# Performance work log

Measured on AMD Instinct MI355X. Metric: run time of the kernel, lower is better.

## Reference

```python
import jax, jax.numpy as jnp
import numpy as np

B, S, D, H = 2, 2048, 1024, 16  # batch, seq_len, model dim, heads


def setup_inputs() -> dict:
    key = jax.random.key(0)
    ks = jax.random.split(key, 5)
    return {
        "x": jax.random.normal(ks[0], (B, S, D), jnp.float32),
        "idx": jax.random.randint(ks[1], (B,), 0, S),
        "weight": jnp.float32(0.5),
        "attn_forcing": 1,  # static python flag
        "w_qkv": jax.random.normal(ks[2], (D, 3 * D), jnp.float32) * 0.02,
        "b_qkv": jnp.zeros((3 * D,), jnp.float32),
        "w_proj": jax.random.normal(ks[3], (D, D), jnp.float32) * 0.02,
        "b_proj": jnp.zeros((D,), jnp.float32),
    }


def reference(x, idx, weight, attn_forcing, w_qkv, b_qkv, w_proj, b_proj):
    Bx, Sx, Dm = x.shape
    dh = Dm // H
    # qkv projection (Conv1D: x @ w + b)
    qkv = x @ w_qkv + b_qkv  # [B,S,3D]
    q, k, v = jnp.split(qkv, 3, axis=-1)
    q = q.reshape(Bx, Sx, H, dh).transpose(0, 2, 1, 3)  # [B,H,S,dh]
    k = k.reshape(Bx, Sx, H, dh).transpose(0, 2, 1, 3)
    v = v.reshape(Bx, Sx, H, dh).transpose(0, 2, 1, 3)
    alen = jnp.arange(Sx)
    mask = (alen[None, :] <= alen[:, None]).astype(x.dtype)  # [S,S] causal
    w = jnp.einsum('bhqd,bhkd->bhqk', q, k) / jnp.asarray(np.sqrt(dh), x.dtype)
    w = w * mask + jnp.asarray(-1e9, x.dtype) * (1 - mask)
    w = jax.nn.softmax(w, axis=-1)
    if attn_forcing:
        # post-softmax forcing reweight: positions >= idx scaled by weight, then renorm
        a = jnp.where(alen[None, :] >= idx[:, None], weight, jnp.asarray(1.0, x.dtype))  # [B,S]
        w = w * a[:, None, None, :]
        w = w / jnp.sum(w, axis=-1, keepdims=True)
    out = jnp.einsum('bhqk,bhkd->bhqd', w, v)  # [B,H,S,dh]
    out = out.transpose(0, 2, 1, 3).reshape(Bx, Sx, Dm)  # merge heads
    return out @ w_proj + b_proj
```

## Files before the change

kernel.cpp:

```cpp
#include <hip/hip_runtime.h>


typedef __attribute__((ext_vector_type(8))) short short8;
typedef __attribute__((ext_vector_type(4))) float f32x4;

#define MFMA_B16(a, b, c) __builtin_amdgcn_mfma_f32_16x16x32_bf16(a, b, c, 0, 0, 0)

static __device__ __forceinline__ unsigned short f2bf(float f) {
    union { float f; unsigned int u; } v;
    v.f = f;
    unsigned int r = (v.u + 0x7fffu + ((v.u >> 16) & 1u)) >> 16;
    return (unsigned short)r;
}

static __device__ __forceinline__ unsigned int pk_bf16(float a, float b) {
#if __has_builtin(__builtin_amdgcn_cvt_pk_bf16_f32)
    typedef __bf16 bf2 __attribute__((ext_vector_type(2)));
    union { bf2 v; unsigned int u; } c;
    c.v = __builtin_amdgcn_cvt_pk_bf16_f32(a, b);
    return c.u;
#else
    return (unsigned int)f2bf(a) | ((unsigned int)f2bf(b) << 16);
#endif
}

static __device__ __forceinline__ void gl_lds16(const void* g, void* l) {
    __builtin_amdgcn_global_load_lds(
        (const __attribute__((address_space(1))) unsigned int*)g,
        (__attribute__((address_space(3))) unsigned int*)l, 16, 0, 0);
}

__global__ __launch_bounds__(256) void convert_x_kernel(const float4* __restrict__ x,
                                                        ushort4* __restrict__ xb) {
    int i = blockIdx.x * 256 + threadIdx.x;
    float4 v = x[i];
    ushort4 o;
    o.x = f2bf(v.x); o.y = f2bf(v.y); o.z = f2bf(v.z); o.w = f2bf(v.w);
    xb[i] = o;
}

__global__ __launch_bounds__(256) void transpose_cvt_kernel(const float* __restrict__ in,
                                                            unsigned short* __restrict__ out,
                                                            int R, int C) {
    __shared__ float t[32][33];
    int c0 = blockIdx.x * 32, r0 = blockIdx.y * 32;
    int x = threadIdx.x, y = threadIdx.y;
    #pragma unroll
    for (int yy = y; yy < 32; yy += 8)
        t[yy][x] = in[(size_t)(r0 + yy) * C + (c0 + x)];
    __syncthreads();
    #pragma unroll
    for (int yy = y; yy < 32; yy += 8)
        out[(size_t)(c0 + yy) * R + (r0 + x)] = f2bf(t[x][yy]);
}

__global__ __launch_bounds__(256) void transpose_v_kernel(const unsigned short* __restrict__ v,
                                                          unsigned short* __restrict__ vT) {
    __shared__ unsigned short t[32][33];
    int d0 = blockIdx.x * 32, s0 = blockIdx.y * 32, bh = blockIdx.z;
    const unsigned short* vb = v + (size_t)bh * 2048 * 64;
    unsigned short* vTb = vT + (size_t)bh * 2048 * 64;
    int x = threadIdx.x, y = threadIdx.y;
    #pragma unroll
    for (int yy = y; yy < 32; yy += 8)
        t[yy][x] = vb[(s0 + yy) * 64 + d0 + x];
    __syncthreads();
    #pragma unroll
    for (int yy = y; yy < 32; yy += 8)
        vTb[(d0 + yy) * 2048 + s0 + x] = t[x][yy];
}

__global__ __launch_bounds__(256) void gemm_qkv_kernel(const unsigned short* __restrict__ A,
                                                       const unsigned short* __restrict__ Bt,
                                                       const float* __restrict__ bias,
                                                       unsigned short* __restrict__ q,
                                                       unsigned short* __restrict__ k,
                                                       unsigned short* __restrict__ v) {
    __shared__ unsigned short As[128 * 64];
    __shared__ unsigned short Bs[128 * 64];
    const int tid = threadIdx.x;
    const int lane = tid & 63, wave = tid >> 6;
    const int l15 = lane & 15, quad = lane >> 4;
    const int wm = wave >> 1, wn = wave & 1;
    const int row0 = blockIdx.y * 128, col0 = blockIdx.x * 128;
    const int K = 1024;

    int srow[4], scol[4], sdst[4];
    #pragma unroll
    for (int h = 0; h < 4; ++h) {
        int D = h * 256 + wave * 64 + lane;
        srow[h] = D >> 3;
        scol[h] = ((D & 7) ^ (srow[h] & 7)) * 8;
        sdst[h] = (h * 256 + wave * 64) * 8;
    }

    f32x4 acc[4][4] = {};

    for (int kt = 0; kt < K; kt += 64) {
        #pragma unroll
        for (int h = 0; h < 4; ++h) {
            gl_lds16(&A[(size_t)(row0 + srow[h]) * K + kt + scol[h]], &As[sdst[h]]);
            gl_lds16(&Bt[(size_t)(col0 + srow[h]) * K + kt + scol[h]], &Bs[sdst[h]]);
        }
        __syncthreads();
        #pragma unroll
        for (int kk = 0; kk < 2; ++kk) {
            short8 af[4], bf[4];
            #pragma unroll
            for (int i = 0; i < 4; ++i) {
                int r = wm * 64 + i * 16 + l15;
                af[i] = *(const short8*)&As[r * 64 + (((kk * 4 + quad) ^ (r & 7)) * 8)];
            }
            #pragma unroll
            for (int j = 0; j < 4; ++j) {
                int r = wn * 64 + j * 16 + l15;
                bf[j] = *(const short8*)&Bs[r * 64 + (((kk * 4 + quad) ^ (r & 7)) * 8)];
            }
            #pragma unroll
            for (int i = 0; i < 4; ++i)
                #pragma unroll
                for (int j = 0; j < 4; ++j)
                    acc[i][j] = MFMA_B16(af[i], bf[j], acc[i][j]);
        }
        __syncthreads();
    }

    #pragma unroll
    for (int i = 0; i < 4; ++i)
        #pragma unroll
        for (int j = 0; j < 4; ++j)
            #pragma unroll
            for (int r = 0; r < 4; ++r) {
                int row = row0 + wm * 64 + i * 16 + quad * 4 + r;
                int col = col0 + wn * 64 + j * 16 + l15;
                float val = acc[i][j][r] + bias[col];
                int which = col >> 10, rem = col & 1023;
                int hh = rem >> 6, d = rem & 63;
                int b = row >> 11, s = row & 2047;
                size_t o = ((size_t)((b * 16 + hh) * 2048 + s)) * 64 + d;
                if (which == 0) q[o] = f2bf(val * 0.125f);
                else if (which == 1) k[o] = f2bf(val);
                else v[o] = f2bf(val);
            }
}

__global__ __launch_bounds__(256) void gemm_proj_kernel(const unsigned short* __restrict__ A,
                                                        const unsigned short* __restrict__ Bt,
                                                        const float* __restrict__ bias,
                                                        float* __restrict__ out) {
    __shared__ unsigned short As[128 * 64];
    __shared__ unsigned short Bs[64 * 64];
    const int tid = threadIdx.x;
    const int lane = tid & 63, wave = tid >> 6;
    const int l15 = lane & 15, quad = lane >> 4;
    const int wm = wave >> 1, wn = wave & 1;
    const int row0 = blockIdx.y * 128, col0 = blockIdx.x * 64;
    const int K = 1024;

    int srow[4], scol[4], sdst[4];
    #pragma unroll
    for (int h = 0; h < 4; ++h) {
        int D = h * 256 + wave * 64 + lane;
        srow[h] = D >> 3;
        scol[h] = ((D & 7) ^ (srow[h] & 7)) * 8;
        sdst[h] = (h * 256 + wave * 64) * 8;
    }

    f32x4 acc[4][2] = {};

    for (int kt = 0; kt < K; kt += 64) {
        #pragma unroll
        for (int h = 0; h < 4; ++h)
            gl_lds16(&A[(size_t)(row0 + srow[h]) * K + kt + scol[h]], &As[sdst[h]]);
        #pragma unroll
        for (int h = 0; h < 2; ++h)
            gl_lds16(&Bt[(size_t)(col0 + srow[h]) * K + kt + scol[h]], &Bs[sdst[h]]);
        __syncthreads();
        #pragma unroll
        for (int kk = 0; kk < 2; ++kk) {
            short8 af[4], bf[2];
            #pragma unroll
            for (int i = 0; i < 4; ++i) {
                int r = wm * 64 + i * 16 + l15;
                af[i] = *(const short8*)&As[r * 64 + (((kk * 4 + quad) ^ (r & 7)) * 8)];
            }
            #pragma unroll
            for (int j = 0; j < 2; ++j) {
                int r = wn * 32 + j * 16 + l15;
                bf[j] = *(const short8*)&Bs[r * 64 + (((kk * 4 + quad) ^ (r & 7)) * 8)];
            }
            #pragma unroll
            for (int i = 0; i < 4; ++i)
                #pragma unroll
                for (int j = 0; j < 2; ++j)
                    acc[i][j] = MFMA_B16(af[i], bf[j], acc[i][j]);
        }
        __syncthreads();
    }

    #pragma unroll
    for (int i = 0; i < 4; ++i)
        #pragma unroll
        for (int j = 0; j < 2; ++j)
            #pragma unroll
            for (int r = 0; r < 4; ++r) {
                int row = row0 + wm * 64 + i * 16 + quad * 4 + r;
                int col = col0 + wn * 32 + j * 16 + l15;
                out[(size_t)row * 1024 + col] = acc[i][j][r] + bias[col];
            }
}

__global__ __launch_bounds__(256) void attn_kernel(const unsigned short* __restrict__ Q,
                                                   const unsigned short* __restrict__ Kg,
                                                   const unsigned short* __restrict__ Vt,
                                                   const int* __restrict__ idx,
                                                   const float* __restrict__ weight,
                                                   const int* __restrict__ forcing,
                                                   unsigned short* __restrict__ O) {
    __shared__ unsigned short Ks[2][4096];
    __shared__ unsigned short Vs[2][4096];

    const int tid = threadIdx.x;
    const int lane = tid & 63, wave = tid >> 6;
    const int l15 = lane & 15, quad = lane >> 4;
    const int bid = blockIdx.x;
    const int u = bid >> 5, a = u & 7, qg = u >> 3;
    const int t = (qg == 0) ? (31 - a) : (qg == 1) ? (16 + a) : (qg == 2) ? (15 - a) : a;
    const int bh = bid & 31;
    const int b = bh >> 4, hh = bh & 15;
    const unsigned short* Qb = Q + (size_t)bh * 2048 * 64;
    const unsigned short* Kh = Kg + (size_t)bh * 2048 * 64;
    const unsigned short* Vh = Vt + (size_t)bh * 2048 * 64;

    const int idxb = idx[b];
    const float wgt = (forcing[0] != 0) ? weight[0] : 1.0f;

    const int L0 = wave * 128 + lane;
    const int rS = L0 >> 3;
    const int cS = (L0 & 7) ^ (rS & 7);
    const int ldsOffJ0 = (wave * 128) * 8;
    const int ldsOffJ1 = (wave * 128 + 64) * 8;

    const int q0 = t * 64 + wave * 16;
    const int qrow = q0 + l15;

    short8 aq0 = *(const short8*)&Qb[(q0 + l15) * 64 + quad * 8];
    short8 aq1 = *(const short8*)&Qb[(q0 + l15) * 64 + 32 + quad * 8];

    float m = -3.0e38f, l = 0.0f;
    f32x4 o[4] = {};

    const int nkb = t + 1;

    {
        const unsigned short* kg = Kh + (size_t)rS * 64 + cS * 8;
        const unsigned short* vg = Vh + (size_t)rS * 2048 + cS * 8;
        gl_lds16(kg,            &Ks[0][ldsOffJ0]);
        gl_lds16(kg + 8 * 64,   &Ks[0][ldsOffJ1]);
        gl_lds16(vg,            &Vs[0][ldsOffJ0]);
        gl_lds16(vg + 8 * 2048, &Vs[0][ldsOffJ1]);
    }
    __syncthreads();

    for (int kb = 0; kb < nkb; ++kb) {
        const int cur = kb & 1;
        const int kbase = kb * 64;
        if (kb + 1 < nkb) {
            const int nb = kbase + 64;
            const unsigned short* kg = Kh + (size_t)(nb + rS) * 64 + cS * 8;
            const unsigned short* vg = Vh + (size_t)rS * 2048 + nb + cS * 8;
            gl_lds16(kg,            &Ks[cur ^ 1][ldsOffJ0]);
            gl_lds16(kg + 8 * 64,   &Ks[cur ^ 1][ldsOffJ1]);
            gl_lds16(vg,            &Vs[cur ^ 1][ldsOffJ0]);
            gl_lds16(vg + 8 * 2048, &Vs[cur ^ 1][ldsOffJ1]);
        }

        f32x4 sT[4];
        #pragma unroll
        for (int kt = 0; kt < 4; ++kt) {
            const int row = kt * 16 + l15;
            short8 k0 = *(const short8*)&Ks[cur][row * 64 + ((quad ^ (row & 7)) * 8)];
            short8 k1 = *(const short8*)&Ks[cur][row * 64 + (((4 + quad) ^ (row & 7)) * 8)];
            f32x4 z = {};
            z = MFMA_B16(k0, aq0, z);
            z = MFMA_B16(k1, aq1, z);
            sT[kt] = z;
        }

        if (kb == t) {
            #pragma unroll
            for (int kt = 0; kt < 4; ++kt)
                #pragma unroll
                for (int r = 0; r < 4; ++r)
                    if (kbase + kt * 16 + quad * 4 + r > qrow) sT[kt][r] = -3.0e38f;
        }

        float mloc = fmaxf(fmaxf(fmaxf(sT[0][0], sT[0][1]), fmaxf(sT[0][2], sT[0][3])),
                           fmaxf(fmaxf(sT[1][0], sT[1][1]), fmaxf(sT[1][2], sT[1][3])));
        mloc = fmaxf(mloc, fmaxf(fmaxf(fmaxf(sT[2][0], sT[2][1]), fmaxf(sT[2][2], sT[2][3])),
                                 fmaxf(fmaxf(sT[3][0], sT[3][1]), fmaxf(sT[3][2], sT[3][3]))));
        mloc = fmaxf(mloc, __shfl_xor(mloc, 16));
        mloc = fmaxf(mloc, __shfl_xor(mloc, 32));
        const float mnew = fmaxf(m, mloc);
        const float alpha = __expf(m - mnew);
        m = mnew;

        #pragma unroll
        for (int kt = 0; kt < 4; ++kt)
            #pragma unroll
            for (int r = 0; r < 4; ++r)
                sT[kt][r] = __expf(sT[kt][r] - mnew);
        if (kbase >= idxb) {
            #pragma unroll
            for (int kt = 0; kt < 4; ++kt)
                #pragma unroll
                for (int r = 0; r < 4; ++r) sT[kt][r] *= wgt;
        } else if (kbase + 63 >= idxb) {
            #pragma unroll
            for (int kt = 0; kt < 4; ++kt)
                #pragma unroll
                for (int r = 0; r < 4; ++r)
                    if (kbase + kt * 16 + quad * 4 + r >= idxb) sT[kt][r] *= wgt;
        }

        float rs = ((sT[0][0] + sT[0][1]) + (sT[0][2] + sT[0][3])) +
                   ((sT[1][0] + sT[1][1]) + (sT[1][2] + sT[1][3])) +
                   ((sT[2][0] + sT[2][1]) + (sT[2][2] + sT[2][3])) +
                   ((sT[3][0] + sT[3][1]) + (sT[3][2] + sT[3][3]));
        rs += __shfl_xor(rs, 16);
        rs += __shfl_xor(rs, 32);
        l = l * alpha + rs;

        #pragma unroll
        for (int dt = 0; dt < 4; ++dt) {
            f32x4 tt = o[dt];
            #pragma unroll
            for (int r = 0; r < 4; ++r) tt[r] *= alpha;
            o[dt] = tt;
        }

        unsigned int plo[4], phi[4];
        #pragma unroll
        for (int kt = 0; kt < 4; ++kt) {
            plo[kt] = pk_bf16(sT[kt][0], sT[kt][1]);
            phi[kt] = pk_bf16(sT[kt][2], sT[kt][3]);
        }

        #pragma unroll
        for (int ka = 0; ka < 2; ++ka) {
            const int srcA = ((quad & 1) * 32) + l15;
            const int srcB = srcA + 16;
            unsigned int tA0 = __shfl(plo[ka * 2], srcA), tA1 = __shfl(plo[ka * 2 + 1], srcA);
            unsigned int hA0 = __shfl(phi[ka * 2], srcA), hA1 = __shfl(phi[ka * 2 + 1], srcA);
            unsigned int tB0 = __shfl(plo[ka * 2], srcB), tB1 = __shfl(plo[ka * 2 + 1], srcB);
            unsigned int hB0 = __shfl(phi[ka * 2], srcB), hB1 = __shfl(phi[ka * 2 + 1], srcB);
            const bool hi = quad >= 2;
            union { short8 v; unsigned int u[4]; } pf;
            pf.u[0] = hi ? tA1 : tA0;
            pf.u[1] = hi ? hA1 : hA0;
            pf.u[2] = hi ? tB1 : tB0;
            pf.u[3] = hi ? hB1 : hB0;
            #pragma unroll
            for (int dt = 0; dt < 4; ++dt) {
                const int row = dt * 16 + l15;
                short8 vf = *(const short8*)&Vs[cur][row * 64 + (((ka * 4 + quad) ^ (row & 7)) * 8)];
                o[dt] = MFMA_B16(vf, pf.v, o[dt]);
            }
        }

        __syncthreads();
    }

    const float inv = 1.0f / l;
    unsigned short* sc = &Ks[0][0] + wave * 1152;
    #pragma unroll
    for (int dt = 0; dt < 4; ++dt)
        #pragma unroll
        for (int r = 0; r < 4; ++r)
            sc[l15 * 72 + dt * 16 + quad * 4 + r] = f2bf(o[dt][r] * inv);
    const size_t rowoff = ((size_t)(b * 2048 + q0 + l15)) * 1024 + hh * 64;
    #pragma unroll
    for (int h = 0; h < 2; ++h) {
        short8 v8 = *(const short8*)&sc[l15 * 72 + quad * 16 + h * 8];
        *(short8*)&O[rowoff + quad * 16 + h * 8] = v8;
    }
}

extern "C" void kernel_launch(void* const* d_in, const int* in_sizes, int n_in,
                              void* d_out, int out_size, void* d_ws, size_t ws_size,
                              hipStream_t stream) {
    const float* x        = (const float*)d_in[0];
    const int*   idx      = (const int*)d_in[1];
    const float* weight   = (const float*)d_in[2];
    const int*   forcing  = (const int*)d_in[3];
    const float* w_qkv    = (const float*)d_in[4];
    const float* b_qkv    = (const float*)d_in[5];
    const float* w_proj   = (const float*)d_in[6];
    const float* b_proj   = (const float*)d_in[7];
    float* out = (float*)d_out;

    char* ws = (char*)d_ws;
    unsigned short* xb      = (unsigned short*)(ws);
    unsigned short* wqkvT   = (unsigned short*)(ws + 8388608);
    unsigned short* wprojT  = (unsigned short*)(ws + 14680064);
    unsigned short* qbuf    = (unsigned short*)(ws + 16777216);
    unsigned short* kbuf    = (unsigned short*)(ws + 25165824);
    unsigned short* vbuf    = (unsigned short*)(ws + 33554432);
    unsigned short* vTbuf   = (unsigned short*)(ws + 41943040);
    unsigned short* attn_out = xb;

    convert_x_kernel<<<4096, 256, 0, stream>>>((const float4*)x, (ushort4*)xb);
    transpose_cvt_kernel<<<dim3(96, 32), dim3(32, 8), 0, stream>>>(w_qkv, wqkvT, 1024, 3072);
    transpose_cvt_kernel<<<dim3(32, 32), dim3(32, 8), 0, stream>>>(w_proj, wprojT, 1024, 1024);
    gemm_qkv_kernel<<<dim3(24, 32), 256, 0, stream>>>(xb, wqkvT, b_qkv, qbuf, kbuf, vbuf);
    transpose_v_kernel<<<dim3(2, 64, 32), dim3(32, 8), 0, stream>>>(vbuf, vTbuf);
    attn_kernel<<<1024, 256, 0, stream>>>(qbuf, kbuf, vTbuf, idx, weight, forcing, attn_out);
    gemm_proj_kernel<<<dim3(16, 32), 256, 0, stream>>>(attn_out, wprojT, b_proj, out);
}
```

Before: 213.5 us.

## Split long causal query tiles across two blocks and add combine kernel

Query tiles 16-31, which have the longest causal KV ranges, are each split into two blocks that process halves of the KV range. The halves write unnormalized bf16 partial outputs plus running max and sum to workspace, and a new combine kernel merges them with a log-sum-exp rescale. The goal is to balance load and raise block count to cut tail imbalance on the attention kernel. The PV product also switches from shuffle-based P redistribution to 16x16x16 bf16 MFMAs fed directly from registers, which removes the shuffles. The cost is an extra kernel launch, extra global traffic for the partials, and some precision loss from storing partials in bf16.

```diff
diff --git a/kernel.cpp b/kernel.cpp
--- a/kernel.cpp
+++ b/kernel.cpp
@@ -2,15 +2,34 @@
 
 
 typedef __attribute__((ext_vector_type(8))) short short8;
+typedef __attribute__((ext_vector_type(4))) short s4v;
 typedef __attribute__((ext_vector_type(4))) float f32x4;
 
 #define MFMA_B16(a, b, c) __builtin_amdgcn_mfma_f32_16x16x32_bf16(a, b, c, 0, 0, 0)
+
+#if __has_builtin(__builtin_amdgcn_mfma_f32_16x16x16_bf16_1k)
+static __device__ __forceinline__ f32x4 MFMA16(s4v a, s4v b, f32x4 c) {
+    return __builtin_amdgcn_mfma_f32_16x16x16_bf16_1k(a, b, c, 0, 0, 0);
+}
+#else
+static __device__ __forceinline__ f32x4 MFMA16(s4v a, s4v b, f32x4 c) {
+    short8 a8 = {a[0], a[1], a[2], a[3], 0, 0, 0, 0};
+    short8 b8 = {b[0], b[1], b[2], b[3], 0, 0, 0, 0};
+    return MFMA_B16(a8, b8, c);
+}
+#endif
 
 static __device__ __forceinline__ unsigned short f2bf(float f) {
     union { float f; unsigned int u; } v;
     v.f = f;
     unsigned int r = (v.u + 0x7fffu + ((v.u >> 16) & 1u)) >> 16;
     return (unsigned short)r;
+}
+
+static __device__ __forceinline__ float bf2f(unsigned short h) {
+    union { unsigned int u; float f; } v;
+    v.u = ((unsigned int)h) << 16;
+    return v.f;
 }
 
 static __device__ __forceinline__ unsigned int pk_bf16(float a, float b) {
@@ -216,17 +235,36 @@
                                                    const int* __restrict__ idx,
                                                    const float* __restrict__ weight,
                                                    const int* __restrict__ forcing,
-                                                   unsigned short* __restrict__ O) {
+                                                   unsigned short* __restrict__ O,
+                                                   unsigned short* __restrict__ opart,
+                                                   float* __restrict__ ml) {
     __shared__ unsigned short Ks[2][4096];
     __shared__ unsigned short Vs[2][4096];
 
     const int tid = threadIdx.x;
     const int lane = tid & 63, wave = tid >> 6;
     const int l15 = lane & 15, quad = lane >> 4;
+
     const int bid = blockIdx.x;
-    const int u = bid >> 5, a = u & 7, qg = u >> 3;
-    const int t = (qg == 0) ? (31 - a) : (qg == 1) ? (16 + a) : (qg == 2) ? (15 - a) : a;
-    const int bh = bid & 31;
+    int t, bh, kb0, kb1, pi;
+    bool split;
+    if (bid < 1024) {
+        t = 31 - (bid >> 6);
+        const int rem = bid & 63;
+        bh = rem >> 1;
+        const int half = rem & 1;
+        const int nkb = t + 1, mid = (nkb + 1) >> 1;
+        kb0 = half ? mid : 0;
+        kb1 = half ? nkb : mid;
+        split = true;
+        pi = ((t - 16) * 32 + bh) * 2 + half;
+    } else {
+        const int g = bid - 1024;
+        t = 15 - (g >> 5);
+        bh = g & 31;
+        kb0 = 0; kb1 = t + 1;
+        split = false; pi = 0;
+    }
     const int b = bh >> 4, hh = bh & 15;
     const unsigned short* Qb = Q + (size_t)bh * 2048 * 64;
     const unsigned short* Kh = Kg + (size_t)bh * 2048 * 64;
@@ -250,11 +288,9 @@
     float m = -3.0e38f, l = 0.0f;
     f32x4 o[4] = {};
 
-    const int nkb = t + 1;
-
     {
-        const unsigned short* kg = Kh + (size_t)rS * 64 + cS * 8;
-        const unsigned short* vg = Vh + (size_t)rS * 2048 + cS * 8;
+        const unsigned short* kg = Kh + (size_t)(kb0 * 64 + rS) * 64 + cS * 8;
+        const unsigned short* vg = Vh + (size_t)rS * 2048 + kb0 * 64 + cS * 8;
         gl_lds16(kg,            &Ks[0][ldsOffJ0]);
         gl_lds16(kg + 8 * 64,   &Ks[0][ldsOffJ1]);
         gl_lds16(vg,            &Vs[0][ldsOffJ0]);
@@ -262,10 +298,10 @@
     }
     __syncthreads();
 
-    for (int kb = 0; kb < nkb; ++kb) {
-        const int cur = kb & 1;
+    for (int kb = kb0; kb < kb1; ++kb) {
+        const int cur = (kb - kb0) & 1;
         const int kbase = kb * 64;
-        if (kb + 1 < nkb) {
+        if (kb + 1 < kb1) {
             const int nb = kbase + 64;
             const unsigned short* kg = Kh + (size_t)(nb + rS) * 64 + cS * 8;
             const unsigned short* vg = Vh + (size_t)rS * 2048 + nb + cS * 8;
@@ -339,50 +375,81 @@
             o[dt] = tt;
         }
 
-        unsigned int plo[4], phi[4];
+        s4v pf[4];
         #pragma unroll
         for (int kt = 0; kt < 4; ++kt) {
-            plo[kt] = pk_bf16(sT[kt][0], sT[kt][1]);
-            phi[kt] = pk_bf16(sT[kt][2], sT[kt][3]);
-        }
-
-        #pragma unroll
-        for (int ka = 0; ka < 2; ++ka) {
-            const int srcA = ((quad & 1) * 32) + l15;
-            const int srcB = srcA + 16;
-            unsigned int tA0 = __shfl(plo[ka * 2], srcA), tA1 = __shfl(plo[ka * 2 + 1], srcA);
-            unsigned int hA0 = __shfl(phi[ka * 2], srcA), hA1 = __shfl(phi[ka * 2 + 1], srcA);
-            unsigned int tB0 = __shfl(plo[ka * 2], srcB), tB1 = __shfl(plo[ka * 2 + 1], srcB);
-            unsigned int hB0 = __shfl(phi[ka * 2], srcB), hB1 = __shfl(phi[ka * 2 + 1], srcB);
-            const bool hi = quad >= 2;
-            union { short8 v; unsigned int u[4]; } pf;
-            pf.u[0] = hi ? tA1 : tA0;
-            pf.u[1] = hi ? hA1 : hA0;
-            pf.u[2] = hi ? tB1 : tB0;
-            pf.u[3] = hi ? hB1 : hB0;
-            #pragma unroll
-            for (int dt = 0; dt < 4; ++dt) {
-                const int row = dt * 16 + l15;
-                short8 vf = *(const short8*)&Vs[cur][row * 64 + (((ka * 4 + quad) ^ (row & 7)) * 8)];
-                o[dt] = MFMA_B16(vf, pf.v, o[dt]);
-            }
+            union { unsigned int u[2]; s4v v; } pu;
+            pu.u[0] = pk_bf16(sT[kt][0], sT[kt][1]);
+            pu.u[1] = pk_bf16(sT[kt][2], sT[kt][3]);
+            pf[kt] = pu.v;
+        }
+
+        #pragma unroll
+        for (int dt = 0; dt < 4; ++dt) {
+            const int row = dt * 16 + l15;
+            f32x4 oo = o[dt];
+            #pragma unroll
+            for (int kt = 0; kt < 4; ++kt) {
+                s4v vf = *(const s4v*)&Vs[cur][row * 64 +
+                          (((2 * kt + (quad >> 1)) ^ (row & 7)) * 8 + (quad & 1) * 4)];
+                oo = MFMA16(vf, pf[kt], oo);
+            }
+            o[dt] = oo;
         }
 
         __syncthreads();
     }
 
-    const float inv = 1.0f / l;
-    unsigned short* sc = &Ks[0][0] + wave * 1152;
-    #pragma unroll
-    for (int dt = 0; dt < 4; ++dt)
-        #pragma unroll
-        for (int r = 0; r < 4; ++r)
-            sc[l15 * 72 + dt * 16 + quad * 4 + r] = f2bf(o[dt][r] * inv);
-    const size_t rowoff = ((size_t)(b * 2048 + q0 + l15)) * 1024 + hh * 64;
-    #pragma unroll
-    for (int h = 0; h < 2; ++h) {
-        short8 v8 = *(const short8*)&sc[l15 * 72 + quad * 16 + h * 8];
-        *(short8*)&O[rowoff + quad * 16 + h * 8] = v8;
+    if (!split) {
+        const float inv = 1.0f / l;
+        unsigned short* sc = &Ks[0][0] + wave * 1152;
+        #pragma unroll
+        for (int dt = 0; dt < 4; ++dt)
+            #pragma unroll
+            for (int r = 0; r < 4; ++r)
+                sc[l15 * 72 + dt * 16 + quad * 4 + r] = f2bf(o[dt][r] * inv);
+        const size_t rowoff = ((size_t)(b * 2048 + q0 + l15)) * 1024 + hh * 64;
+        #pragma unroll
+        for (int h = 0; h < 2; ++h) {
+            short8 v8 = *(const short8*)&sc[l15 * 72 + quad * 16 + h * 8];
+            *(short8*)&O[rowoff + quad * 16 + h * 8] = v8;
+        }
+    } else {
+        unsigned short* op = opart + (size_t)pi * 4096;
+        #pragma unroll
+        for (int dt = 0; dt < 4; ++dt)
+            #pragma unroll
+            for (int r = 0; r < 4; ++r)
+                op[(dt * 16 + quad * 4 + r) * 64 + wave * 16 + l15] = f2bf(o[dt][r]);
+        if (quad == 0) {
+            ml[pi * 128 + wave * 16 + l15] = m;
+            ml[pi * 128 + 64 + wave * 16 + l15] = l;
+        }
+    }
+}
+
+__global__ __launch_bounds__(256) void attn_combine_kernel(const unsigned short* __restrict__ opart,
+                                                           const float* __restrict__ ml,
+                                                           unsigned short* __restrict__ O) {
+    const int blk = blockIdx.x;
+    const int t = 16 + (blk >> 5);
+    const int bh = blk & 31;
+    const int b = bh >> 4, hh = bh & 15;
+    const int pi0 = ((t - 16) * 32 + bh) * 2, pi1 = pi0 + 1;
+    const int d = threadIdx.x & 63;
+    const int qo = threadIdx.x >> 6;
+    #pragma unroll
+    for (int r = 0; r < 16; ++r) {
+        const int qrow = r * 4 + qo;
+        const float m0 = ml[pi0 * 128 + qrow], l0 = ml[pi0 * 128 + 64 + qrow];
+        const float m1 = ml[pi1 * 128 + qrow], l1 = ml[pi1 * 128 + 64 + qrow];
+        const float mm = fmaxf(m0, m1);
+        const float e0 = __expf(m0 - mm), e1 = __expf(m1 - mm);
+        const float inv = 1.0f / (l0 * e0 + l1 * e1);
+        const float o0 = bf2f(opart[(size_t)pi0 * 4096 + d * 64 + qrow]);
+        const float o1 = bf2f(opart[(size_t)pi1 * 4096 + d * 64 + qrow]);
+        O[((size_t)(b * 2048 + t * 64 + qrow)) * 1024 + hh * 64 + d] =
+            f2bf((o0 * e0 + o1 * e1) * inv);
     }
 }
 
@@ -408,12 +475,16 @@
     unsigned short* vbuf    = (unsigned short*)(ws + 33554432);
     unsigned short* vTbuf   = (unsigned short*)(ws + 41943040);
     unsigned short* attn_out = xb;
+    unsigned short* opart    = vbuf;
+    float*          mlbuf    = (float*)wqkvT;
 
     convert_x_kernel<<<4096, 256, 0, stream>>>((const float4*)x, (ushort4*)xb);
     transpose_cvt_kernel<<<dim3(96, 32), dim3(32, 8), 0, stream>>>(w_qkv, wqkvT, 1024, 3072);
     transpose_cvt_kernel<<<dim3(32, 32), dim3(32, 8), 0, stream>>>(w_proj, wprojT, 1024, 1024);
     gemm_qkv_kernel<<<dim3(24, 32), 256, 0, stream>>>(xb, wqkvT, b_qkv, qbuf, kbuf, vbuf);
     transpose_v_kernel<<<dim3(2, 64, 32), dim3(32, 8), 0, stream>>>(vbuf, vTbuf);
-    attn_kernel<<<1024, 256, 0, stream>>>(qbuf, kbuf, vTbuf, idx, weight, forcing, attn_out);
+    attn_kernel<<<1536, 256, 0, stream>>>(qbuf, kbuf, vTbuf, idx, weight, forcing,
+                                          attn_out, opart, mlbuf);
+    attn_combine_kernel<<<512, 256, 0, stream>>>(opart, mlbuf, attn_out);
     gemm_proj_kernel<<<dim3(16, 32), 256, 0, stream>>>(attn_out, wprojT, b_proj, out);
 }
```

New measurement: 227.4 us. 1.07x slower.
